# Kernel optimization log

Measured on AMD Instinct MI355X. Metric: run time of the kernel, lower is better.

The kernel has to match this reference:

```python
import jax, jax.numpy as jnp
import numpy as np
from functools import partial

D_MODEL, N_HEADS, D_FF, KSIZE = 512, 8, 2048, 31
B, S = 8, 1024
EPS = 1e-5

def layer_norm(x, g, b):
    m = jnp.mean(x, axis=-1, keepdims=True)
    v = jnp.mean(jnp.square(x - m), axis=-1, keepdims=True)
    return (x - m) * jax.lax.rsqrt(v + EPS) * g + b

def ffn(x, ln_g, ln_b, w1, b1, w2, b2):
    h = layer_norm(x, ln_g, ln_b)
    h = jax.nn.silu(h @ w1 + b1) @ w2 + b2
    return x + 0.5 * h

def mhsa(x, ln_g, ln_b, wq, bq, wk, bk, wv, bv, wo, bo):
    b_, s_, d_ = x.shape
    dk = d_ // N_HEADS
    h = layer_norm(x, ln_g, ln_b)
    def heads(y):  # (B,S,D) -> (B,H,S,dk)
        return y.reshape(b_, s_, N_HEADS, dk).transpose(0, 2, 1, 3)
    Q, K, V = heads(h @ wq + bq), heads(h @ wk + bk), heads(h @ wv + bv)
    scores = jnp.einsum('bhqd,bhkd->bhqk', Q, K) / jnp.sqrt(jnp.float32(dk)).astype(x.dtype)
    attn = jax.nn.softmax(scores, axis=-1)
    ctx = jnp.einsum('bhqk,bhkd->bhqd', attn, V)
    ctx = ctx.transpose(0, 2, 1, 3).reshape(b_, s_, d_)
    return x + (ctx @ wo + bo)

def conv_module(x, ln_g, ln_b, pw1_w, pw1_b, dw_w, dw_b, bn_g, bn_b, bn_mean, bn_var, pw2_w, pw2_b):
    h = layer_norm(x, ln_g, ln_b)           # (B,S,D)
    h = h @ pw1_w + pw1_b                   # (B,S,2D) pointwise conv1 (k=1)
    a, g = jnp.split(h, 2, axis=-1)
    h = a * jax.nn.sigmoid(g)               # GLU over channel dim
    hc = h.transpose(0, 2, 1)               # (B,D,S)
    # depthwise conv: kernel (D,1,K), groups=D, SAME padding (K odd)
    hc = jax.lax.conv_general_dilated(
        hc, dw_w, window_strides=(1,), padding='SAME',
        dimension_numbers=('NCH', 'OIH', 'NCH'),
        feature_group_count=D_MODEL) + dw_b[None, :, None]
    # BatchNorm1d (eval mode, running stats)
    hc = (hc - bn_mean[None, :, None]) * jax.lax.rsqrt(bn_var + EPS)[None, :, None]
    hc = hc * bn_g[None, :, None] + bn_b[None, :, None]
    hc = jax.nn.silu(hc)
    hc = jnp.einsum('bcs,co->bos', hc, pw2_w) + pw2_b[None, :, None]  # pointwise conv2
    return x + hc.transpose(0, 2, 1)


def setup_inputs() -> dict:
    key = jax.random.key(0)
    ks = iter(jax.random.split(key, 48))
    def w(shape, scale=0.02):
        return (jax.random.normal(next(ks), shape, dtype=jnp.float32) * scale)
    d, f = D_MODEL, D_FF
    inp = {
        'x': jax.random.normal(next(ks), (B, S, d), dtype=jnp.float32),
        # FFN1
        'ffn1_ln_g': jnp.ones((d,)), 'ffn1_ln_b': jnp.zeros((d,)),
        'ffn1_w1': w((d, f)), 'ffn1_b1': jnp.zeros((f,)),
        'ffn1_w2': w((f, d)), 'ffn1_b2': jnp.zeros((d,)),
        # MHSA
        'mhsa_ln_g': jnp.ones((d,)), 'mhsa_ln_b': jnp.zeros((d,)),
        'wq': w((d, d)), 'bq': jnp.zeros((d,)),
        'wk': w((d, d)), 'bk': jnp.zeros((d,)),
        'wv': w((d, d)), 'bv': jnp.zeros((d,)),
        'wo': w((d, d)), 'bo': jnp.zeros((d,)),
        # Conv module
        'conv_ln_g': jnp.ones((d,)), 'conv_ln_b': jnp.zeros((d,)),
        'pw1_w': w((d, 2 * d)), 'pw1_b': jnp.zeros((2 * d,)),
        'dw_w': w((d, 1, KSIZE)), 'dw_b': jnp.zeros((d,)),
        'bn_g': jnp.ones((d,)), 'bn_b': jnp.zeros((d,)),
        'bn_mean': jnp.zeros((d,)), 'bn_var': jnp.ones((d,)),
        'pw2_w': w((d, d)), 'pw2_b': jnp.zeros((d,)),
        # FFN2
        'ffn2_ln_g': jnp.ones((d,)), 'ffn2_ln_b': jnp.zeros((d,)),
        'ffn2_w1': w((d, f)), 'ffn2_b1': jnp.zeros((f,)),
        'ffn2_w2': w((f, d)), 'ffn2_b2': jnp.zeros((d,)),
        # Final LN
        'final_ln_g': jnp.ones((d,)), 'final_ln_b': jnp.zeros((d,)),
    }
    return inp


def reference(x,
              ffn1_ln_g, ffn1_ln_b, ffn1_w1, ffn1_b1, ffn1_w2, ffn1_b2,
              mhsa_ln_g, mhsa_ln_b, wq, bq, wk, bk, wv, bv, wo, bo,
              conv_ln_g, conv_ln_b, pw1_w, pw1_b, dw_w, dw_b,
              bn_g, bn_b, bn_mean, bn_var, pw2_w, pw2_b,
              ffn2_ln_g, ffn2_ln_b, ffn2_w1, ffn2_b1, ffn2_w2, ffn2_b2,
              final_ln_g, final_ln_b):
    h = ffn(x, ffn1_ln_g, ffn1_ln_b, ffn1_w1, ffn1_b1, ffn1_w2, ffn1_b2)
    h = mhsa(h, mhsa_ln_g, mhsa_ln_b, wq, bq, wk, bk, wv, bv, wo, bo)
    h = conv_module(h, conv_ln_g, conv_ln_b, pw1_w, pw1_b, dw_w, dw_b,
                    bn_g, bn_b, bn_mean, bn_var, pw2_w, pw2_b)
    h = ffn(h, ffn2_ln_g, ffn2_ln_b, ffn2_w1, ffn2_b1, ffn2_w2, ffn2_b2)
    return layer_norm(h, final_ln_g, final_ln_b)
```

## Files before the change

### kernel.cpp

```cpp
#include <hip/hip_runtime.h>
#include <hip/hip_bf16.h>
#include <cstddef>

typedef __hip_bfloat16 bf16;
typedef __attribute__((ext_vector_type(8))) short bf16x8;
typedef __attribute__((ext_vector_type(4))) float f32x4;
typedef __attribute__((ext_vector_type(2))) unsigned int u32x2;

static __device__ __forceinline__ float b2f(bf16 v) { return __bfloat162float(v); }
static __device__ __forceinline__ bf16 f2b(float v) { return __float2bfloat16(v); }
static __device__ __forceinline__ float bits2f(unsigned short u) {
    union { unsigned int i; float f; } c; c.i = ((unsigned int)u) << 16; return c.f;
}
static __device__ __forceinline__ unsigned int f2bu(float v) {
    union { bf16 b; unsigned short u; } c; c.b = f2b(v); return (unsigned int)c.u;
}
static __device__ __forceinline__ float ldx(const void* p, size_t i, bool isbf) {
    return isbf ? b2f(((const bf16*)p)[i]) : ((const float*)p)[i];
}
#define GLOAD_LDS16(g, l)                                                            \
    __builtin_amdgcn_global_load_lds((const __attribute__((address_space(1))) unsigned int*)(g), \
                                     (__attribute__((address_space(3))) unsigned int*)(l), 16, 0, 0)

#define LN_EPS 1e-5f

__global__ void detect_kernel(const void* ones, int* flag) {
    unsigned int w = *(const unsigned int*)ones;
    *flag = (w == 0x3F803F80u) ? 1 : 0;
}

__global__ void to_f32_kernel(const void* x, float* __restrict__ y, int n8, const int* flag) {
    bool isbf = (*flag != 0);
    int i = blockIdx.x * blockDim.x + threadIdx.x;
    if (i >= n8) return;
    size_t base = (size_t)i * 8;
    if (isbf) {
        bf16x8 xv = *(const bf16x8*)((const bf16*)x + base);
#pragma unroll
        for (int u = 0; u < 8; ++u) y[base + u] = bits2f((unsigned short)xv[u]);
    } else {
        f32x4 a = *(const f32x4*)((const float*)x + base);
        f32x4 b = *(const f32x4*)((const float*)x + base + 4);
        *(f32x4*)(y + base) = a;
        *(f32x4*)(y + base + 4) = b;
    }
}

__global__ __launch_bounds__(256) void transpose_kernel(const void* __restrict__ W,
                                                        bf16* __restrict__ Wt,
                                                        int K, int M, const int* flag) {
    bool isbf = (*flag != 0);
    __shared__ float ts[32][33];
    int kt0 = blockIdx.x * 32, mt0 = blockIdx.y * 32;
    int x = threadIdx.x, y = threadIdx.y;
    for (int yy = y; yy < 32; yy += 8)
        ts[yy][x] = ldx(W, (size_t)(kt0 + yy) * M + mt0 + x, isbf);
    __syncthreads();
    for (int yy = y; yy < 32; yy += 8)
        Wt[(size_t)(mt0 + yy) * K + kt0 + x] = f2b(ts[x][yy]);
}

__global__ void bpack_kernel(const void* bq, const void* bk, const void* bv,
                             void* out, const int* flag) {
    bool isbf = (*flag != 0);
    int i = blockIdx.x * blockDim.x + threadIdx.x;
    if (i >= 1536) return;
    const void* src = (i < 512) ? bq : ((i < 1024) ? bk : bv);
    float v = ldx(src, i & 511, isbf);
    if (isbf) ((bf16*)out)[i] = f2b(v);
    else      ((float*)out)[i] = v;
}

__global__ __launch_bounds__(256) void vtrans_kernel(const bf16* __restrict__ P,
                                                     bf16* __restrict__ Vt) {
    __shared__ bf16 t[32][33];
    int s0 = blockIdx.x * 32, c0 = blockIdx.y * 32, b = blockIdx.z;
    int x = threadIdx.x, y = threadIdx.y;
    const bf16* Pb = P + (size_t)b * 1024 * 1536 + 1024;
    bf16* Vtb = Vt + (size_t)b * 512 * 1024;
    for (int yy = y; yy < 32; yy += 8)
        t[yy][x] = Pb[(size_t)(s0 + yy) * 1536 + c0 + x];
    __syncthreads();
    for (int yy = y; yy < 32; yy += 8)
        Vtb[(size_t)(c0 + yy) * 1024 + s0 + x] = t[x][yy];
}

__global__ void glu_kernel(const bf16* __restrict__ u, bf16* __restrict__ o, int n8) {
    int i = blockIdx.x * blockDim.x + threadIdx.x;
    if (i >= n8) return;
    size_t base = (size_t)i * 8;
    int t = (int)(base >> 9), c = (int)(base & 511);
    bf16x8 av = *(const bf16x8*)(u + (size_t)t * 1024 + c);
    bf16x8 gv = *(const bf16x8*)(u + (size_t)t * 1024 + 512 + c);
    __attribute__((aligned(16))) bf16 ov[8];
#pragma unroll
    for (int k = 0; k < 8; ++k) {
        float a = bits2f((unsigned short)av[k]);
        float g = bits2f((unsigned short)gv[k]);
        ov[k] = f2b(a / (1.f + __expf(-g)));
    }
    *(bf16x8*)(o + base) = *(bf16x8*)ov;
}

__global__ __launch_bounds__(256) void ln_kernel(const float* __restrict__ X,
                                                 const void* __restrict__ g,
                                                 const void* __restrict__ b,
                                                 bf16* __restrict__ O, const int* flag) {
    bool isbf = (*flag != 0);
    int tid = threadIdx.x, lane = tid & 63, wid = tid >> 6;
    int t = blockIdx.x * 4 + wid;
    const float* x = X + (size_t)t * 512 + lane * 8;
    __attribute__((aligned(16))) float v[8];
    *(f32x4*)&v[0] = *(const f32x4*)x;
    *(f32x4*)&v[4] = *(const f32x4*)(x + 4);
    float s = 0.f, q = 0.f;
#pragma unroll
    for (int u = 0; u < 8; ++u) { s += v[u]; q += v[u] * v[u]; }
#pragma unroll
    for (int m = 1; m < 64; m <<= 1) { s += __shfl_xor(s, m, 64); q += __shfl_xor(q, m, 64); }
    float mean = s * (1.f / 512.f);
    float var  = q * (1.f / 512.f) - mean * mean;
    float sc = rsqrtf(var + LN_EPS);
    __attribute__((aligned(16))) bf16 ov[8];
#pragma unroll
    for (int u = 0; u < 8; ++u)
        ov[u] = f2b((v[u] - mean) * sc * ldx(g, lane * 8 + u, isbf) + ldx(b, lane * 8 + u, isbf));
    *(bf16x8*)(O + (size_t)t * 512 + lane * 8) = *(bf16x8*)ov;
}

__global__ __launch_bounds__(256) void ln_out_kernel(const float* __restrict__ X,
                                                     const void* __restrict__ g,
                                                     const void* __restrict__ b,
                                                     void* __restrict__ O, const int* flag) {
    bool isbf = (*flag != 0);
    int tid = threadIdx.x, lane = tid & 63, wid = tid >> 6;
    int t = blockIdx.x * 4 + wid;
    const float* x = X + (size_t)t * 512 + lane * 8;
    __attribute__((aligned(16))) float v[8];
    *(f32x4*)&v[0] = *(const f32x4*)x;
    *(f32x4*)&v[4] = *(const f32x4*)(x + 4);
    float s = 0.f, q = 0.f;
#pragma unroll
    for (int u = 0; u < 8; ++u) { s += v[u]; q += v[u] * v[u]; }
#pragma unroll
    for (int m = 1; m < 64; m <<= 1) { s += __shfl_xor(s, m, 64); q += __shfl_xor(q, m, 64); }
    float mean = s * (1.f / 512.f);
    float var  = q * (1.f / 512.f) - mean * mean;
    float sc = rsqrtf(var + LN_EPS);
    float r[8];
#pragma unroll
    for (int u = 0; u < 8; ++u)
        r[u] = (v[u] - mean) * sc * ldx(g, lane * 8 + u, isbf) + ldx(b, lane * 8 + u, isbf);
    size_t off = (size_t)t * 512 + lane * 8;
    if (isbf) {
        __attribute__((aligned(16))) bf16 ov[8];
#pragma unroll
        for (int u = 0; u < 8; ++u) ov[u] = f2b(r[u]);
        *(bf16x8*)((bf16*)O + off) = *(bf16x8*)ov;
    } else {
        *(f32x4*)((float*)O + off) = *(f32x4*)&r[0];
        *(f32x4*)((float*)O + off + 4) = *(f32x4*)&r[4];
    }
}

template <int ACT, int RESADD, int BM>
__global__ __launch_bounds__(256) void mgemm_kernel(const bf16* __restrict__ A,
                                                    const bf16* __restrict__ Wt,
                                                    const void* __restrict__ bias,
                                                    bf16* __restrict__ Cb,
                                                    float* __restrict__ res, float alpha,
                                                    int lda, int K, int M, const int* flag) {
    constexpr int MI = BM / 32;
    bool isbf = (*flag != 0);
    __shared__ short As[2][BM * 32];
    __shared__ short Bs[2][128 * 32];
    int tid = threadIdx.x;
    int rowBase = blockIdx.y * BM, colBase = blockIdx.x * 128;
    int ll = tid & 63, wv = tid >> 6;
    int wr = (wv & 1) * (BM / 2), wc = (wv >> 1) * 64;
    int lRow = ll & 15, quad = ll >> 4;

    int sR16 = ll >> 2;
    int kseg = (ll & 3) ^ ((ll >> 3) & 3);
    int segF = quad ^ ((lRow >> 1) & 3);

    int nSteps = K >> 5;

    f32x4 acc[MI][4] = {};

    auto STAGE = [&](int buf, int k0) {
#pragma unroll
        for (int j = 0; j < BM / 64; ++j) {
            int rT = wv * (BM / 4) + j * 16;
            const bf16* ga = A + (size_t)(rowBase + rT + sR16) * lda + k0 + kseg * 8;
            GLOAD_LDS16(ga, &As[buf][rT * 32]);
        }
#pragma unroll
        for (int j = 0; j < 2; ++j) {
            int rT = wv * 32 + j * 16;
            const bf16* gb = Wt + (size_t)(colBase + rT + sR16) * K + k0 + kseg * 8;
            GLOAD_LDS16(gb, &Bs[buf][rT * 32]);
        }
    };

    STAGE(0, 0);
    __syncthreads();
    for (int it = 0; it < nSteps; ++it) {
        int cur = it & 1;
        if (it + 1 < nSteps) STAGE(cur ^ 1, (it + 1) * 32);
        bf16x8 af[MI], bfv[4];
#pragma unroll
        for (int i = 0; i < MI; ++i)
            af[i]  = *(const bf16x8*)&As[cur][(wr + i * 16 + lRow) * 32 + segF * 8];
#pragma unroll
        for (int j = 0; j < 4; ++j)
            bfv[j] = *(const bf16x8*)&Bs[cur][(wc + j * 16 + lRow) * 32 + segF * 8];
#pragma unroll
        for (int i = 0; i < MI; ++i)
#pragma unroll
            for (int j = 0; j < 4; ++j)
                acc[i][j] = __builtin_amdgcn_mfma_f32_16x16x32_bf16(af[i], bfv[j], acc[i][j], 0, 0, 0);
        __syncthreads();
    }

#pragma unroll
    for (int j = 0; j < 4; ++j) {
        int col = colBase + wc + j * 16 + lRow;
        float bv = ldx(bias, col, isbf);
#pragma unroll
        for (int i = 0; i < MI; ++i) {
            int r0 = rowBase + wr + i * 16 + quad * 4;
#pragma unroll
            for (int r = 0; r < 4; ++r) {
                float v = acc[i][j][r] + bv;
                if (ACT == 1) v = v / (1.f + __expf(-v));
                int row = r0 + r;
                if (RESADD) res[(size_t)row * 512 + col] += alpha * v;
                else        Cb[(size_t)row * M + col] = f2b(v);
            }
        }
    }
}

__global__ __launch_bounds__(256) void fattn_kernel(bf16* __restrict__ QO,
                                                    const bf16* __restrict__ Vt) {
    __shared__ short Ks[2][64 * 64];
    __shared__ short Vs[2][64 * 64];
    int tid = threadIdx.x, wid = tid >> 6, ll = tid & 63;
    int n = ll & 15, quad = ll >> 4;
    int id = blockIdx.x;
    int ng = gridDim.x >> 4;
    int g = id % ng, j = id / ng;
    int h = g & 7, b = g >> 3;
    size_t rowB = (size_t)b * 1024;
    int q0 = j * 64 + wid * 16;

    const bf16* Qb = QO + rowB * 1536 + h * 64;
    bf16x8 qf0 = *(const bf16x8*)(Qb + (size_t)(q0 + n) * 1536 + quad * 8);
    bf16x8 qf1 = *(const bf16x8*)(Qb + (size_t)(q0 + n) * 1536 + 32 + quad * 8);

    const bf16* Kb = QO + rowB * 1536 + 512 + h * 64;
    const bf16* Vb = Vt + (size_t)b * 512 * 1024 + (size_t)(h * 64) * 1024;

    int rr = ll >> 3;
    int ch = (ll & 7) ^ rr;

    float l = 0.f;
    f32x4 oacc[4] = {};
    int idxA = (((quad & 1) * 32) + n) * 4;
    int idxB = idxA + 64;
    bool hiC = (quad >= 2);
    int nx = n & 7;
    int sl0 = (quad ^ nx) * 8;
    int sl1 = sl0 ^ (4 * 8);

    auto STAGE = [&](int buf, int k0) {
#pragma unroll
        for (int i2 = 0; i2 < 2; ++i2) {
            int r0 = wid * 16 + i2 * 8;
            const bf16* gk = Kb + (size_t)(k0 + r0 + rr) * 1536 + ch * 8;
            GLOAD_LDS16(gk, &Ks[buf][r0 * 64]);
            const bf16* gv = Vb + (size_t)(r0 + rr) * 1024 + k0 + ch * 8;
            GLOAD_LDS16(gv, &Vs[buf][r0 * 64]);
        }
    };

    auto COMPUTE = [&](const short* Kc, const short* Vc) {
#pragma unroll
        for (int s = 0; s < 2; ++s) {
            const short* kb0 = Kc + (s * 32 + n) * 64;
            const short* kb1 = kb0 + 16 * 64;
            f32x4 s0 = {}, s1 = {};
            s0 = __builtin_amdgcn_mfma_f32_16x16x32_bf16(*(const bf16x8*)(kb0 + sl0), qf0, s0, 0, 0, 0);
            s0 = __builtin_amdgcn_mfma_f32_16x16x32_bf16(*(const bf16x8*)(kb0 + sl1), qf1, s0, 0, 0, 0);
            s1 = __builtin_amdgcn_mfma_f32_16x16x32_bf16(*(const bf16x8*)(kb1 + sl0), qf0, s1, 0, 0, 0);
            s1 = __builtin_amdgcn_mfma_f32_16x16x32_bf16(*(const bf16x8*)(kb1 + sl1), qf1, s1, 0, 0, 0);

            float p0[4], p1[4];
#pragma unroll
            for (int r = 0; r < 4; ++r) {
                p0[r] = __expf(s0[r] * 0.125f);
                p1[r] = __expf(s1[r] * 0.125f);
                l += p0[r] + p1[r];
            }

            int p0d0 = (int)(f2bu(p0[0]) | (f2bu(p0[1]) << 16));
            int p0d1 = (int)(f2bu(p0[2]) | (f2bu(p0[3]) << 16));
            int p1d0 = (int)(f2bu(p1[0]) | (f2bu(p1[1]) << 16));
            int p1d1 = (int)(f2bu(p1[2]) | (f2bu(p1[3]) << 16));
            int a0 = __builtin_amdgcn_ds_bpermute(idxA, p0d0);
            int a1 = __builtin_amdgcn_ds_bpermute(idxA, p0d1);
            int a2 = __builtin_amdgcn_ds_bpermute(idxB, p0d0);
            int a3 = __builtin_amdgcn_ds_bpermute(idxB, p0d1);
            int c0 = __builtin_amdgcn_ds_bpermute(idxA, p1d0);
            int c1 = __builtin_amdgcn_ds_bpermute(idxA, p1d1);
            int c2 = __builtin_amdgcn_ds_bpermute(idxB, p1d0);
            int c3 = __builtin_amdgcn_ds_bpermute(idxB, p1d1);
            union { int d[4]; bf16x8 v; } bf;
            bf.d[0] = hiC ? c0 : a0;
            bf.d[1] = hiC ? c1 : a1;
            bf.d[2] = hiC ? c2 : a2;
            bf.d[3] = hiC ? c3 : a3;

            int vsl = ((s * 4 + quad) ^ nx) * 8;
#pragma unroll
            for (int g2 = 0; g2 < 4; ++g2) {
                const short* vp = Vc + (g2 * 16 + n) * 64 + vsl;
                oacc[g2] = __builtin_amdgcn_mfma_f32_16x16x32_bf16(*(const bf16x8*)vp, bf.v, oacc[g2], 0, 0, 0);
            }
        }
    };

    STAGE(0, 0);
    __syncthreads();
    for (int it = 0; it < 16; it += 2) {
        if (it + 1 < 16) STAGE(1, (it + 1) * 64);
        COMPUTE(&Ks[0][0], &Vs[0][0]);
        __syncthreads();
        if (it + 2 < 16) STAGE(0, (it + 2) * 64);
        COMPUTE(&Ks[1][0], &Vs[1][0]);
        __syncthreads();
    }

    l += __shfl_xor(l, 16, 64);
    l += __shfl_xor(l, 32, 64);
    float linv = 1.f / l;
    bf16* op = QO + (rowB + q0 + n) * 1536 + h * 64 + quad * 4;
#pragma unroll
    for (int g2 = 0; g2 < 4; ++g2) {
        union { bf16 b4[4]; u32x2 w; } ou;
#pragma unroll
        for (int r = 0; r < 4; ++r) ou.b4[r] = f2b(oacc[g2][r] * linv);
        *(u32x2*)(op + g2 * 16) = ou.w;
    }
}

__global__ void dwprep_kernel(const void* __restrict__ w, const void* __restrict__ dwb,
                              const void* __restrict__ bng, const void* __restrict__ bnb,
                              const void* __restrict__ bnm, const void* __restrict__ bnv,
                              bf16* __restrict__ wT, float* __restrict__ scl,
                              float* __restrict__ sft, const int* flag) {
    bool isbf = (*flag != 0);
    int c = blockIdx.x * blockDim.x + threadIdx.x;
    if (c >= 512) return;
    for (int k = 0; k < 31; ++k) wT[k * 512 + c] = f2b(ldx(w, (size_t)c * 31 + k, isbf));
    float s = ldx(bng, c, isbf) * rsqrtf(ldx(bnv, c, isbf) + LN_EPS);
    scl[c] = s;
    sft[c] = (ldx(dwb, c, isbf) - ldx(bnm, c, isbf)) * s + ldx(bnb, c, isbf);
}

__global__ __launch_bounds__(256) void dwconv_kernel(const bf16* __restrict__ X,
                                                     const bf16* __restrict__ wT,
                                                     const float* __restrict__ scl,
                                                     const float* __restrict__ sft,
                                                     bf16* __restrict__ Out) {
    __shared__ bf16 wl[31 * 512];
    __shared__ float sl[512], fl[512];
    int tid = threadIdx.x;
    for (int i = tid; i < (31 * 512) / 8; i += 256)
        *(bf16x8*)&wl[i * 8] = *(const bf16x8*)&wT[i * 8];
    sl[tid] = scl[tid]; sl[tid + 256] = scl[tid + 256];
    fl[tid] = sft[tid]; fl[tid + 256] = sft[tid + 256];
    __syncthreads();

    int lane = tid & 63, sg = tid >> 6;
    int c = lane * 8;
    size_t bOff = (size_t)blockIdx.y * 1024 * 512;
    int sb = blockIdx.x * 16 + sg * 4;

    float acc[4][8] = {};
    for (int kk = 0; kk < 34; ++kk) {
        int sp = sb + kk - 15;
        if (sp < 0 || sp >= 1024) continue;
        bf16x8 xr = *(const bf16x8*)(X + bOff + (size_t)sp * 512 + c);
        float xv[8];
#pragma unroll
        for (int u = 0; u < 8; ++u) xv[u] = bits2f((unsigned short)xr[u]);
#pragma unroll
        for (int o = 0; o < 4; ++o) {
            int kw = kk - o;
            if (kw < 0 || kw > 30) continue;
            bf16x8 wv8 = *(const bf16x8*)&wl[kw * 512 + c];
#pragma unroll
            for (int u = 0; u < 8; ++u) acc[o][u] += xv[u] * bits2f((unsigned short)wv8[u]);
        }
    }
#pragma unroll
    for (int o = 0; o < 4; ++o) {
        __attribute__((aligned(16))) bf16 ov[8];
#pragma unroll
        for (int u = 0; u < 8; ++u) {
            float v = acc[o][u] * sl[c + u] + fl[c + u];
            v = v / (1.f + __expf(-v));
            ov[u] = f2b(v);
        }
        *(bf16x8*)(Out + bOff + (size_t)(sb + o) * 512 + c) = *(bf16x8*)ov;
    }
}

extern "C" void kernel_launch(void* const* d_in, const int* in_sizes, int n_in,
                              void* d_out, int out_size, void* d_ws, size_t ws_size,
                              hipStream_t stream) {
    const int B = 8, S = 1024, D = 512, F = 2048, H = 8;
    const int N = B * S;
    const size_t ND = (size_t)N * D;
    if (n_in < 37) return;

    int idx = 0;
    const void* x          = d_in[idx++];
    const void* ffn1_ln_g  = d_in[idx++];
    const void* ffn1_ln_b  = d_in[idx++];
    const void* ffn1_w1    = d_in[idx++];
    const void* ffn1_b1    = d_in[idx++];
    const void* ffn1_w2    = d_in[idx++];
    const void* ffn1_b2    = d_in[idx++];
    const void* mhsa_ln_g  = d_in[idx++];
    const void* mhsa_ln_b  = d_in[idx++];
    const void* wq         = d_in[idx++];
    const void* bq         = d_in[idx++];
    const void* wk         = d_in[idx++];
    const void* bk         = d_in[idx++];
    const void* wv         = d_in[idx++];
    const void* bv         = d_in[idx++];
    const void* wo         = d_in[idx++];
    const void* bo         = d_in[idx++];
    const void* conv_ln_g  = d_in[idx++];
    const void* conv_ln_b  = d_in[idx++];
    const void* pw1_w      = d_in[idx++];
    const void* pw1_b      = d_in[idx++];
    const void* dw_w       = d_in[idx++];
    const void* dw_b       = d_in[idx++];
    const void* bn_g       = d_in[idx++];
    const void* bn_b       = d_in[idx++];
    const void* bn_mean    = d_in[idx++];
    const void* bn_var     = d_in[idx++];
    const void* pw2_w      = d_in[idx++];
    const void* pw2_b      = d_in[idx++];
    const void* ffn2_ln_g  = d_in[idx++];
    const void* ffn2_ln_b  = d_in[idx++];
    const void* ffn2_w1    = d_in[idx++];
    const void* ffn2_b1    = d_in[idx++];
    const void* ffn2_w2    = d_in[idx++];
    const void* ffn2_b2    = d_in[idx++];
    const void* final_ln_g = d_in[idx++];
    const void* final_ln_b = d_in[idx++];

    const size_t MB = 1024 * 1024;
    char* wsb  = (char*)d_ws;
    int*  flag = (int*)wsb;
    float* res = (float*)(wsb + 1024);
    bf16*  wt  = (bf16*)(wsb + 1024 + ND * 4);
    char*  dwr = wsb + 1024 + ND * 4 + 4 * MB;
    bf16*  dwT  = (bf16*)dwr;
    float* dscl = (float*)(dwr + 32768);
    float* dsft = dscl + 512;
    void*  qkvB = (void*)(dwr + 40960);
    char*  scr = dwr + 65536;
    size_t base = 1024 + ND * 4 + 4 * MB + 65536;
    size_t scrB = (ws_size > base) ? ws_size - base : 0;
    int ffnRows = (scrB >= 32 * MB) ? 8192 : ((scrB >= 8 * MB) ? 2048 : 1024);
    int bI      = (scrB >= 32 * MB) ? 8    : ((scrB >= 8 * MB) ? 2    : 1);
    int cI      = (scrB >= 32 * MB) ? 8    : ((scrB >= 8 * MB) ? 2    : 1);

    bf16* h = (bf16*)d_out;

    detect_kernel<<<1, 1, 0, stream>>>(ffn1_ln_g, flag);
    to_f32_kernel<<<(int)(ND / 8 / 256), 256, 0, stream>>>(x, res, (int)(ND / 8), flag);

    auto run_ffn = [&](const void* lg, const void* lb, const void* w1, const void* b1,
                       const void* w2, const void* b2) {
        bf16* w1t = wt;
        bf16* w2t = wt + (size_t)D * F;
        transpose_kernel<<<dim3(D / 32, F / 32), dim3(32, 8), 0, stream>>>(w1, w1t, D, F, flag);
        transpose_kernel<<<dim3(F / 32, D / 32), dim3(32, 8), 0, stream>>>(w2, w2t, F, D, flag);
        ln_kernel<<<N / 4, 256, 0, stream>>>(res, lg, lb, h, flag);
        bf16* mid = (bf16*)scr;
        for (int r0 = 0; r0 < N; r0 += ffnRows) {
            mgemm_kernel<1, 0, 128><<<dim3(F / 128, ffnRows / 128), 256, 0, stream>>>(
                h + (size_t)r0 * D, w1t, b1, mid, nullptr, 0.f, D, D, F, flag);
            mgemm_kernel<0, 1, 64><<<dim3(D / 128, ffnRows / 64), 256, 0, stream>>>(
                mid, w2t, b2, nullptr, res + (size_t)r0 * D, 0.5f, F, F, D, flag);
        }
    };

    run_ffn(ffn1_ln_g, ffn1_ln_b, ffn1_w1, ffn1_b1, ffn1_w2, ffn1_b2);

    {
        bf16* qt = wt;
        bf16* kt = wt + (size_t)D * D;
        bf16* vt = wt + 2 * (size_t)D * D;
        bf16* ot = wt + 3 * (size_t)D * D;
        transpose_kernel<<<dim3(D / 32, D / 32), dim3(32, 8), 0, stream>>>(wq, qt, D, D, flag);
        transpose_kernel<<<dim3(D / 32, D / 32), dim3(32, 8), 0, stream>>>(wk, kt, D, D, flag);
        transpose_kernel<<<dim3(D / 32, D / 32), dim3(32, 8), 0, stream>>>(wv, vt, D, D, flag);
        transpose_kernel<<<dim3(D / 32, D / 32), dim3(32, 8), 0, stream>>>(wo, ot, D, D, flag);
        bpack_kernel<<<6, 256, 0, stream>>>(bq, bk, bv, qkvB, flag);
        ln_kernel<<<N / 4, 256, 0, stream>>>(res, mhsa_ln_g, mhsa_ln_b, h, flag);
        for (int b = 0; b < B; b += bI) {
            int rows = bI * S;
            bf16* packed = (bf16*)scr;
            bf16* Vt = packed + (size_t)rows * 1536;
            const bf16* Ah = h + (size_t)b * S * D;
            mgemm_kernel<0, 0, 128><<<dim3(1536 / 128, rows / 128), 256, 0, stream>>>(
                Ah, qt, qkvB, packed, nullptr, 0.f, D, D, 1536, flag);
            vtrans_kernel<<<dim3(S / 32, D / 32, bI), dim3(32, 8), 0, stream>>>(packed, Vt);
            fattn_kernel<<<dim3(bI * H * 16), 256, 0, stream>>>(packed, Vt);
            mgemm_kernel<0, 1, 64><<<dim3(D / 128, rows / 64), 256, 0, stream>>>(
                packed, ot, bo, nullptr, res + (size_t)b * S * D, 1.0f, 1536, D, D, flag);
        }
    }

    {
        bf16* p1t = wt;
        bf16* p2t = wt + (size_t)D * 2 * D;
        transpose_kernel<<<dim3(D / 32, (2 * D) / 32), dim3(32, 8), 0, stream>>>(pw1_w, p1t, D, 2 * D, flag);
        transpose_kernel<<<dim3(D / 32, D / 32), dim3(32, 8), 0, stream>>>(pw2_w, p2t, D, D, flag);
        dwprep_kernel<<<2, 256, 0, stream>>>(dw_w, dw_b, bn_g, bn_b, bn_mean, bn_var, dwT, dscl, dsft, flag);
        ln_kernel<<<N / 4, 256, 0, stream>>>(res, conv_ln_g, conv_ln_b, h, flag);
        for (int b = 0; b < B; b += cI) {
            int rows = cI * S;
            bf16* u  = (bf16*)scr;
            bf16* hg = u + (size_t)rows * 2 * D;
            bf16* dw = hg + (size_t)rows * D;
            const bf16* Ah = h + (size_t)b * S * D;
            mgemm_kernel<0, 0, 128><<<dim3((2 * D) / 128, rows / 128), 256, 0, stream>>>(
                Ah, p1t, pw1_b, u, nullptr, 0.f, D, D, 2 * D, flag);
            glu_kernel<<<(rows * D / 8) / 256, 256, 0, stream>>>(u, hg, rows * D / 8);
            dwconv_kernel<<<dim3(S / 16, cI), 256, 0, stream>>>(hg, dwT, dscl, dsft, dw);
            mgemm_kernel<0, 1, 64><<<dim3(D / 128, rows / 64), 256, 0, stream>>>(
                dw, p2t, pw2_b, nullptr, res + (size_t)b * S * D, 1.0f, D, D, D, flag);
        }
    }

    run_ffn(ffn2_ln_g, ffn2_ln_b, ffn2_w1, ffn2_b1, ffn2_w2, ffn2_b2);

    ln_out_kernel<<<N / 4, 256, 0, stream>>>(res, final_ln_g, final_ln_b, d_out, flag);
}
```

Baseline: 570.8 us.

## Deepen GEMM K-tile to 64 with two-stage prefetch and manual waitcnt barriers

Doubles the K-step of the MFMA GEMM tile from 32 to 64, which halves the number of barrier iterations, and changes the LDS swizzle to an 8-chunk XOR layout. Loads are now issued two tiles ahead into the buffer just consumed. Fragments are read into registers before a barrier and the prefetch starts before the MFMAs run. Synchronisation uses explicit s_waitcnt vmcnt counts with raw s_barrier so global-to-LDS loads overlap compute. This doubles LDS usage, which may reduce occupancy, and the hand-set vmcnt values are fragile if the count of loads per stage changes.

```diff
diff --git a/kernel.cpp b/kernel.cpp
--- a/kernel.cpp
+++ b/kernel.cpp
@@ -172,55 +172,75 @@
                                                     int lda, int K, int M, const int* flag) {
     constexpr int MI = BM / 32;
     bool isbf = (*flag != 0);
-    __shared__ short As[2][BM * 32];
-    __shared__ short Bs[2][128 * 32];
+    __shared__ short As[2][BM * 64];
+    __shared__ short Bs[2][128 * 64];
     int tid = threadIdx.x;
     int rowBase = blockIdx.y * BM, colBase = blockIdx.x * 128;
     int ll = tid & 63, wv = tid >> 6;
     int wr = (wv & 1) * (BM / 2), wc = (wv >> 1) * 64;
     int lRow = ll & 15, quad = ll >> 4;
-
-    int sR16 = ll >> 2;
-    int kseg = (ll & 3) ^ ((ll >> 3) & 3);
-    int segF = quad ^ ((lRow >> 1) & 3);
-
-    int nSteps = K >> 5;
+    int rr = ll >> 3;
+    int ch = (ll & 7) ^ rr;
+    int slA = (quad ^ (lRow & 7)) * 8;
+
+    int nSteps = K >> 6;
 
     f32x4 acc[MI][4] = {};
 
     auto STAGE = [&](int buf, int k0) {
 #pragma unroll
-        for (int j = 0; j < BM / 64; ++j) {
-            int rT = wv * (BM / 4) + j * 16;
-            const bf16* ga = A + (size_t)(rowBase + rT + sR16) * lda + k0 + kseg * 8;
-            GLOAD_LDS16(ga, &As[buf][rT * 32]);
-        }
-#pragma unroll
-        for (int j = 0; j < 2; ++j) {
-            int rT = wv * 32 + j * 16;
-            const bf16* gb = Wt + (size_t)(colBase + rT + sR16) * K + k0 + kseg * 8;
-            GLOAD_LDS16(gb, &Bs[buf][rT * 32]);
+        for (int j = 0; j < BM / 32; ++j) {
+            int rT = wv * (BM / 4) + j * 8;
+            const bf16* ga = A + (size_t)(rowBase + rT + rr) * lda + k0 + ch * 8;
+            GLOAD_LDS16(ga, &As[buf][rT * 64]);
+        }
+#pragma unroll
+        for (int j = 0; j < 4; ++j) {
+            int rT = wv * 32 + j * 8;
+            const bf16* gb = Wt + (size_t)(colBase + rT + rr) * K + k0 + ch * 8;
+            GLOAD_LDS16(gb, &Bs[buf][rT * 64]);
         }
     };
 
     STAGE(0, 0);
-    __syncthreads();
+    STAGE(1, 64);
+    if constexpr (BM == 128) asm volatile("s_waitcnt vmcnt(8)" ::: "memory");
+    else                     asm volatile("s_waitcnt vmcnt(6)" ::: "memory");
+    __builtin_amdgcn_s_barrier();
+
     for (int it = 0; it < nSteps; ++it) {
         int cur = it & 1;
-        if (it + 1 < nSteps) STAGE(cur ^ 1, (it + 1) * 32);
-        bf16x8 af[MI], bfv[4];
-#pragma unroll
-        for (int i = 0; i < MI; ++i)
-            af[i]  = *(const bf16x8*)&As[cur][(wr + i * 16 + lRow) * 32 + segF * 8];
-#pragma unroll
-        for (int j = 0; j < 4; ++j)
-            bfv[j] = *(const bf16x8*)&Bs[cur][(wc + j * 16 + lRow) * 32 + segF * 8];
-#pragma unroll
-        for (int i = 0; i < MI; ++i)
+        const short* Ac = &As[cur][0];
+        const short* Bc = &Bs[cur][0];
+        bf16x8 af[2][MI], bfv[2][4];
+#pragma unroll
+        for (int h = 0; h < 2; ++h) {
+            int sl = slA ^ (h * 32);
+#pragma unroll
+            for (int i = 0; i < MI; ++i)
+                af[h][i] = *(const bf16x8*)&Ac[(wr + i * 16 + lRow) * 64 + sl];
 #pragma unroll
             for (int j = 0; j < 4; ++j)
-                acc[i][j] = __builtin_amdgcn_mfma_f32_16x16x32_bf16(af[i], bfv[j], acc[i][j], 0, 0, 0);
-        __syncthreads();
+                bfv[h][j] = *(const bf16x8*)&Bc[(wc + j * 16 + lRow) * 64 + sl];
+        }
+        asm volatile("s_waitcnt lgkmcnt(0)" ::: "memory");
+        __builtin_amdgcn_s_barrier();
+        bool pf = (it + 2 < nSteps);
+        if (pf) STAGE(cur, (it + 2) * 64);
+#pragma unroll
+        for (int h = 0; h < 2; ++h)
+#pragma unroll
+            for (int i = 0; i < MI; ++i)
+#pragma unroll
+                for (int j = 0; j < 4; ++j)
+                    acc[i][j] = __builtin_amdgcn_mfma_f32_16x16x32_bf16(af[h][i], bfv[h][j], acc[i][j], 0, 0, 0);
+        if (pf) {
+            if constexpr (BM == 128) asm volatile("s_waitcnt vmcnt(8)" ::: "memory");
+            else                     asm volatile("s_waitcnt vmcnt(6)" ::: "memory");
+        } else {
+            asm volatile("s_waitcnt vmcnt(0)" ::: "memory");
+        }
+        __builtin_amdgcn_s_barrier();
     }
 
 #pragma unroll
```

After: 542.2 us. 1.05x faster.
